# Kernel tuning notes

Hardware: AMD Instinct MI355X
Metric: run time of the kernel (lower is better)

The kernel has to match this reference:

```python
import jax, jax.numpy as jnp
import numpy as np

H = 12        # attention heads
WIN = 256     # one-sided sliding window (attention_window = 512)
L = 2         # encoder layers in this reference (full model: 12, same structure)
NEG = -1e9


def layer_norm(x, g, b, eps=1e-5):
    m = jnp.mean(x, axis=-1, keepdims=True)
    v = jnp.mean((x - m) ** 2, axis=-1, keepdims=True)
    return (x - m) * jax.lax.rsqrt(v + eps) * g + b


def heads(x):
    B, S, D = x.shape
    return x.reshape(B, S, H, D // H).transpose(0, 2, 1, 3)  # [B,H,S,Dh]


def overlap_chunks(x, w):
    # x: [B,H,S,D] -> [B,H,C,3w,D]; chunk c = keys/values seen by queries [c*w,(c+1)*w)
    B, Hh, S, D = x.shape
    xp = jnp.pad(x, ((0, 0), (0, 0), (w, w), (0, 0))).reshape(B, Hh, S // w + 2, w, D)
    return jnp.concatenate([xp[:, :, :-2], xp[:, :, 1:-1], xp[:, :, 2:]], axis=3)


def encoder_layer(x, mask, p):
    (Wq, bq, Wk, bk, Wv, bv, Wqg, bqg, Wkg, bkg, Wvg, bvg,
     Wo, bo, g1, b1n, W1, bf1, W2, bf2, g2, b2n) = p
    B, S, D = x.shape
    Dh = D // H
    w = WIN
    C = S // w
    scale = 1.0 / np.sqrt(Dh)
    q = heads(x @ Wq + bq)
    k = heads(x @ Wk + bk)
    v = heads(x @ Wv + bv)
    # --- sliding-window (banded) attention, chunked: each query chunk sees 3 key chunks ---
    qc = q.reshape(B, H, C, w, Dh)
    k3 = overlap_chunks(k, w)
    v3 = overlap_chunks(v, w)
    scores = jnp.einsum('bhcqd,bhckd->bhcqk', qc, k3) * scale  # [B,H,C,w,3w]
    qi = jnp.arange(w)[:, None]
    kr = jnp.arange(3 * w)[None, :] - w                       # key offset rel. to chunk start
    band = jnp.abs(kr - qi) <= w                              # [w,3w] |rel pos| <= w
    kpos = jnp.arange(C)[:, None] * w + (jnp.arange(3 * w) - w)[None, :]  # [C,3w] abs key idx
    inrange = (kpos >= 0) & (kpos < S)
    mp = jnp.pad(mask, ((0, 0), (w, w))).reshape(B, C + 2, w)
    m3 = jnp.concatenate([mp[:, :-2], mp[:, 1:-1], mp[:, 2:]], axis=2)  # [B,C,3w]
    loc_mask = band[None, :, :] & inrange[:, None, :]         # [C,w,3w]
    valid = loc_mask[None, None] & (m3 > 0)[:, None, :, None, :]
    scores = jnp.where(valid, scores, NEG)
    sloc = scores.reshape(B, H, S, 3 * w)
    # every token also attends to the global token (position 0)
    gsc = jnp.einsum('bhsd,bhd->bhs', q, k[:, :, 0]) * scale  # [B,H,S]
    attn = jax.nn.softmax(jnp.concatenate([sloc, gsc[..., None]], axis=-1), axis=-1)
    aloc = attn[..., :3 * w].reshape(B, H, C, w, 3 * w)
    ag = attn[..., -1]                                        # [B,H,S]
    out = jnp.einsum('bhcqk,bhckd->bhcqd', aloc, v3).reshape(B, H, S, Dh)
    out = out + ag[..., None] * v[:, :, 0][:, :, None, :]
    # --- global token full attention with separate global projections ---
    qg = heads(x @ Wqg + bqg)[:, :, 0]                        # [B,H,Dh]
    kg = heads(x @ Wkg + bkg)
    vg = heads(x @ Wvg + bvg)
    gs = jnp.where(mask[:, None, :] > 0,
                   jnp.einsum('bhd,bhsd->bhs', qg, kg) * scale, NEG)
    og = jnp.einsum('bhs,bhsd->bhd', jax.nn.softmax(gs, axis=-1), vg)
    out = out.at[:, :, 0].set(og)
    h = out.transpose(0, 2, 1, 3).reshape(B, S, D) @ Wo + bo
    x = layer_norm(x + h, g1, b1n)
    f = jax.nn.gelu(x @ W1 + bf1) @ W2 + bf2
    return layer_norm(x + f, g2, b2n)


def forward(input_ids, attention_mask, word_emb, pos_emb, ln_e_g, ln_e_b,
            Wq, bq, Wk, bk, Wv, bv, Wqg, bqg, Wkg, bkg, Wvg, bvg, Wo, bo,
            ln1_g, ln1_b, W1, bf1, W2, bf2, ln2_g, ln2_b, Wp, bp, Wc, bc):
    B, S = input_ids.shape
    x = word_emb[input_ids] + pos_emb[:S][None]
    x = layer_norm(x, ln_e_g, ln_e_b)
    for l in range(L):
        p = (Wq[l], bq[l], Wk[l], bk[l], Wv[l], bv[l], Wqg[l], bqg[l],
             Wkg[l], bkg[l], Wvg[l], bvg[l], Wo[l], bo[l], ln1_g[l], ln1_b[l],
             W1[l], bf1[l], W2[l], bf2[l], ln2_g[l], ln2_b[l])
        x = encoder_layer(x, attention_mask, p)
    pooled = jnp.tanh(x[:, 0] @ Wp + bp)   # BERT-style pooler on CLS
    return pooled @ Wc + bc


def setup_inputs() -> dict:
    B, S, D, V, F, NL = 2, 4096, 768, 50265, 3072, 2
    keys = iter(jax.random.split(jax.random.key(0), 64))
    def w(shape, s=0.02):
        return (jax.random.normal(next(keys), shape, jnp.float32) * s)
    inp = {
        'input_ids': jax.random.randint(next(keys), (B, S), 0, V),
        'attention_mask': jnp.ones((B, S), jnp.int32),
        'word_emb': w((V, D)), 'pos_emb': w((S, D)),
        'ln_e_g': jnp.ones((D,), jnp.float32), 'ln_e_b': jnp.zeros((D,), jnp.float32),
        'Wq': w((L, D, D)), 'bq': jnp.zeros((L, D), jnp.float32),
        'Wk': w((L, D, D)), 'bk': jnp.zeros((L, D), jnp.float32),
        'Wv': w((L, D, D)), 'bv': jnp.zeros((L, D), jnp.float32),
        'Wqg': w((L, D, D)), 'bqg': jnp.zeros((L, D), jnp.float32),
        'Wkg': w((L, D, D)), 'bkg': jnp.zeros((L, D), jnp.float32),
        'Wvg': w((L, D, D)), 'bvg': jnp.zeros((L, D), jnp.float32),
        'Wo': w((L, D, D)), 'bo': jnp.zeros((L, D), jnp.float32),
        'ln1_g': jnp.ones((L, D), jnp.float32), 'ln1_b': jnp.zeros((L, D), jnp.float32),
        'W1': w((L, D, F)), 'bf1': jnp.zeros((L, F), jnp.float32),
        'W2': w((L, F, D)), 'bf2': jnp.zeros((L, D), jnp.float32),
        'ln2_g': jnp.ones((L, D), jnp.float32), 'ln2_b': jnp.zeros((L, D), jnp.float32),
        'Wp': w((D, D)), 'bp': jnp.zeros((D,), jnp.float32),
        'Wc': w((D, NL)), 'bc': jnp.zeros((NL,), jnp.float32),
    }
    return inp


def reference(input_ids, attention_mask, word_emb, pos_emb, ln_e_g, ln_e_b,
              Wq, bq, Wk, bk, Wv, bv, Wqg, bqg, Wkg, bkg, Wvg, bvg, Wo, bo,
              ln1_g, ln1_b, W1, bf1, W2, bf2, ln2_g, ln2_b, Wp, bp, Wc, bc):
    return forward(input_ids, attention_mask, word_emb, pos_emb, ln_e_g, ln_e_b,
                   Wq, bq, Wk, bk, Wv, bv, Wqg, bqg, Wkg, bkg, Wvg, bvg, Wo, bo,
                   ln1_g, ln1_b, W1, bf1, W2, bf2, ln2_g, ln2_b, Wp, bp, Wc, bc)
```

## Files before the change

### kernel.cpp

```cpp
#include <hip/hip_runtime.h>
#include <hip/hip_bf16.h>
#include <math.h>

#define BB 2
#define SS 4096
#define DD 768
#define HH 12
#define DHH 64
#define WW 256
#define CC 16
#define FF 3072

typedef __attribute__((ext_vector_type(8))) short bf16x8;
typedef __attribute__((ext_vector_type(4))) float f32x4;

struct TP12 { const float* s[12]; unsigned short* d[12]; };
struct TP4  { const float* s[4];  unsigned short* d[4];  };

__device__ __forceinline__ float gelu_f(float x) {
    float u = 0.7978845608028654f * fmaf(0.044715f * x * x, x, x);
    return x / (1.f + __expf(-2.f * u));
}

__device__ __forceinline__ unsigned short bfb(float f) {
    __hip_bfloat16 h = __float2bfloat16(f);
    return *(unsigned short*)&h;
}

__device__ __forceinline__ float bf2f(unsigned short u) {
    return __uint_as_float(((unsigned int)u) << 16);
}

__device__ __forceinline__ void gload16(const void* g, void* l) {
    __builtin_amdgcn_global_load_lds(
        (const __attribute__((address_space(1))) unsigned int*)g,
        (__attribute__((address_space(3))) unsigned int*)l, 16, 0, 0);
}

__global__ __launch_bounds__(256) void transpose12_k(TP12 p)
{
    __shared__ float t[32][33];
    int z = blockIdx.z;
    const float* Wsrc = p.s[z];
    unsigned short* Wt = p.d[z];
    const int K = DD, N = DD;
    int n0 = blockIdx.x * 32, k0 = blockIdx.y * 32;
    int tx = threadIdx.x & 31, ty = threadIdx.x >> 5;
#pragma unroll
    for (int i = 0; i < 32; i += 8)
        t[ty + i][tx] = Wsrc[(size_t)(k0 + ty + i) * N + n0 + tx];
    __syncthreads();
#pragma unroll
    for (int i = 0; i < 32; i += 8)
        Wt[(size_t)(n0 + ty + i) * K + k0 + tx] = bfb(t[tx][ty + i]);
}

__global__ __launch_bounds__(256) void transposeR4_k(TP4 p)
{
    __shared__ float t[32][33];
    int z = blockIdx.z;
    const float* Wsrc = p.s[z];
    unsigned short* Wt = p.d[z];
    int K, N, n0, k0;
    if (z < 2) { K = DD; N = FF; n0 = blockIdx.x * 32; k0 = blockIdx.y * 32; }
    else { K = FF; N = DD; int cell = blockIdx.y * 96 + blockIdx.x;
           n0 = (cell % 24) * 32; k0 = (cell / 24) * 32; }
    int tx = threadIdx.x & 31, ty = threadIdx.x >> 5;
#pragma unroll
    for (int i = 0; i < 32; i += 8)
        t[ty + i][tx] = Wsrc[(size_t)(k0 + ty + i) * N + n0 + tx];
    __syncthreads();
#pragma unroll
    for (int i = 0; i < 32; i += 8)
        Wt[(size_t)(n0 + ty + i) * K + k0 + tx] = bfb(t[tx][ty + i]);
}

__global__ __launch_bounds__(256) void pack_bias5_k(const float* __restrict__ b0,
        const float* __restrict__ b1, const float* __restrict__ b2,
        const float* __restrict__ b3, const float* __restrict__ b4,
        float* __restrict__ dst)
{
    int gid = blockIdx.x * 256 + threadIdx.x;
    if (gid >= 2 * 5 * DD) return;
    int l = gid / (5 * DD), r = gid % (5 * DD), seg = r / DD, i = r % DD;
    const float* srcs[5] = { b0, b1, b2, b3, b4 };
    dst[gid] = srcs[seg][l * DD + i];
}

__global__ __launch_bounds__(256) void embed_ln_k(const int* __restrict__ ids,
        const float* __restrict__ wemb, const float* __restrict__ pemb,
        const float* __restrict__ g, const float* __restrict__ bta,
        float* __restrict__ x, unsigned short* __restrict__ xbf)
{
    int row = blockIdx.x;
    int s = row & (SS - 1);
    int tid = threadIdx.x;
    int lane = tid & 63, wvi = tid >> 6;
    __shared__ float red[8];
    float4 v = { 0.f, 0.f, 0.f, 0.f };
    if (tid < 192) {
        const float4* we = (const float4*)(wemb + (size_t)ids[row] * DD);
        const float4* pe = (const float4*)(pemb + (size_t)s * DD);
        float4 a = we[tid], b = pe[tid];
        v.x = a.x + b.x; v.y = a.y + b.y; v.z = a.z + b.z; v.w = a.w + b.w;
    }
    float sum = (v.x + v.y) + (v.z + v.w);
    float sq = fmaf(v.x, v.x, fmaf(v.y, v.y, fmaf(v.z, v.z, v.w * v.w)));
#pragma unroll
    for (int o = 1; o < 64; o <<= 1) {
        sum += __shfl_xor(sum, o);
        sq  += __shfl_xor(sq, o);
    }
    if (lane == 0) { red[wvi] = sum; red[4 + wvi] = sq; }
    __syncthreads();
    float S = (red[0] + red[1]) + (red[2] + red[3]);
    float Q = (red[4] + red[5]) + (red[6] + red[7]);
    float mean = S * (1.f / DD);
    float var = Q * (1.f / DD) - mean * mean;
    float rstd = rsqrtf(var + 1e-5f);
    if (tid < 192) {
        float4 gg = ((const float4*)g)[tid];
        float4 bb = ((const float4*)bta)[tid];
        float4 o;
        o.x = (v.x - mean) * rstd * gg.x + bb.x;
        o.y = (v.y - mean) * rstd * gg.y + bb.y;
        o.z = (v.z - mean) * rstd * gg.z + bb.z;
        o.w = (v.w - mean) * rstd * gg.w + bb.w;
        ((float4*)(x + (size_t)row * DD))[tid] = o;
        ushort4 ob = { bfb(o.x), bfb(o.y), bfb(o.z), bfb(o.w) };
        ((ushort4*)(xbf + (size_t)row * DD))[tid] = ob;
    }
}

__global__ __launch_bounds__(256) void add_ln_k(const float* __restrict__ xin,
        const float* __restrict__ hin, const float* __restrict__ g,
        const float* __restrict__ bta, float* __restrict__ xout,
        unsigned short* __restrict__ xbf)
{
    int row = blockIdx.x;
    int tid = threadIdx.x;
    int lane = tid & 63, wvi = tid >> 6;
    __shared__ float red[8];
    float4 v = { 0.f, 0.f, 0.f, 0.f };
    if (tid < 192) {
        float4 a = ((const float4*)(xin + (size_t)row * DD))[tid];
        float4 b = ((const float4*)(hin + (size_t)row * DD))[tid];
        v.x = a.x + b.x; v.y = a.y + b.y; v.z = a.z + b.z; v.w = a.w + b.w;
    }
    float sum = (v.x + v.y) + (v.z + v.w);
    float sq = fmaf(v.x, v.x, fmaf(v.y, v.y, fmaf(v.z, v.z, v.w * v.w)));
#pragma unroll
    for (int o = 1; o < 64; o <<= 1) {
        sum += __shfl_xor(sum, o);
        sq  += __shfl_xor(sq, o);
    }
    if (lane == 0) { red[wvi] = sum; red[4 + wvi] = sq; }
    __syncthreads();
    float S = (red[0] + red[1]) + (red[2] + red[3]);
    float Q = (red[4] + red[5]) + (red[6] + red[7]);
    float mean = S * (1.f / DD);
    float var = Q * (1.f / DD) - mean * mean;
    float rstd = rsqrtf(var + 1e-5f);
    if (tid < 192) {
        float4 gg = ((const float4*)g)[tid];
        float4 bb = ((const float4*)bta)[tid];
        float4 o;
        o.x = (v.x - mean) * rstd * gg.x + bb.x;
        o.y = (v.y - mean) * rstd * gg.y + bb.y;
        o.z = (v.z - mean) * rstd * gg.z + bb.z;
        o.w = (v.w - mean) * rstd * gg.w + bb.w;
        ((float4*)(xout + (size_t)row * DD))[tid] = o;
        ushort4 ob = { bfb(o.x), bfb(o.y), bfb(o.z), bfb(o.w) };
        ((ushort4*)(xbf + (size_t)row * DD))[tid] = ob;
    }
}

template<int OUT_BF16, int ACT_GELU>
__global__ __launch_bounds__(256) void mfma_gemm_k(
        const unsigned short* __restrict__ A,
        const unsigned short* __restrict__ Bt,
        const float* __restrict__ bias,
        void* __restrict__ Cv, int M, int N, int K)
{
    __shared__ short As[2 * 128 * 64];
    __shared__ short Bs[2 * 128 * 64];
    const int tid = threadIdx.x;
    const int lane = tid & 63, wv = tid >> 6;
    int nbx = gridDim.x;
    int nby = gridDim.y;
    int nwg = nbx * nby;
    int lid = blockIdx.y * nbx + blockIdx.x;
    int nid = ((nwg & 7) == 0) ? ((lid & 7) * (nwg >> 3) + (lid >> 3)) : lid;
    const int bm = (nid / nby) * 128, bn = (nid % nby) * 128;
    const int wm = wv >> 1, wn = wv & 1;

    const int srow0 = (tid * 16) >> 7;
    const int sbc   = (tid * 16) & 127;
    const int srcc  = sbc ^ ((srow0 & 7) << 4);
    const int ldst  = tid * 16;
    const char* Ab = (const char*)(A + (size_t)bm * K);
    const char* Bb = (const char*)(Bt + (size_t)bn * K);

    f32x4 acc[4][4];
#pragma unroll
    for (int i = 0; i < 4; i++)
#pragma unroll
        for (int j = 0; j < 4; j++) acc[i][j] = (f32x4){0.f, 0.f, 0.f, 0.f};

    const int lr = lane & 15;
    const int g = lane >> 4;
    const int rswz = (lr & 7) << 4;
    const int NK = K >> 6;

    auto stage = [&](int ib, int t) {
        const int k0 = t << 6;
        char* Ad = (char*)As + ib * 16384;
        char* Bd = (char*)Bs + ib * 16384;
#pragma unroll
        for (int p = 0; p < 4; p++) {
            size_t roff = (size_t)(srow0 + p * 32) * (K * 2) + (size_t)k0 * 2 + srcc;
            gload16(Ab + roff, Ad + p * 4096 + ldst);
            gload16(Bb + roff, Bd + p * 4096 + ldst);
        }
    };

    stage(0, 0);

    int cur = 0;
    for (int t = 0; t < NK; t++) {
        if (t + 1 < NK) {
            stage(cur ^ 1, t + 1);
            asm volatile("s_waitcnt vmcnt(8)" ::: "memory");
        } else {
            asm volatile("s_waitcnt vmcnt(0)" ::: "memory");
        }
        __builtin_amdgcn_sched_barrier(0);
        __builtin_amdgcn_s_barrier();
        __builtin_amdgcn_sched_barrier(0);

        const char* Ar = (const char*)As + cur * 16384;
        const char* Br = (const char*)Bs + cur * 16384;
#pragma unroll
        for (int kk = 0; kk < 2; kk++) {
            int colb = (kk * 64 + g * 16) ^ rswz;
            bf16x8 af[4], bfr[4];
#pragma unroll
            for (int i = 0; i < 4; i++)
                af[i] = *(const bf16x8*)(Ar + (wm * 64 + i * 16 + lr) * 128 + colb);
#pragma unroll
            for (int j = 0; j < 4; j++)
                bfr[j] = *(const bf16x8*)(Br + (wn * 64 + j * 16 + lr) * 128 + colb);
#pragma unroll
            for (int i = 0; i < 4; i++)
#pragma unroll
                for (int j = 0; j < 4; j++)
                    acc[i][j] = __builtin_amdgcn_mfma_f32_16x16x32_bf16(af[i], bfr[j], acc[i][j], 0, 0, 0);
        }
        __builtin_amdgcn_sched_barrier(0);
        __builtin_amdgcn_s_barrier();
        cur ^= 1;
    }

    const int rq = lane >> 4;
#pragma unroll
    for (int j = 0; j < 4; j++) {
        int col = bn + wn * 64 + j * 16 + lr;
        float bv = bias[col];
#pragma unroll
        for (int i = 0; i < 4; i++) {
            int rowb = bm + wm * 64 + i * 16 + rq * 4;
#pragma unroll
            for (int r = 0; r < 4; r++) {
                float o = acc[i][j][r] + bv;
                if (ACT_GELU) o = gelu_f(o);
                if (OUT_BF16)
                    ((unsigned short*)Cv)[(size_t)(rowb + r) * N + col] = bfb(o);
                else
                    ((float*)Cv)[(size_t)(rowb + r) * N + col] = o;
            }
        }
    }
}

__global__ __launch_bounds__(256) void vtrans_k(const unsigned short* __restrict__ packed,
        unsigned short* __restrict__ vt)
{
    int s0 = blockIdx.x * 64, h = blockIdx.y, b = blockIdx.z;
    int tid = threadIdx.x;
    __shared__ unsigned short t[64][72];
    int r = tid >> 3, dc = (tid & 7) * 8;
#pragma unroll
    for (int half = 0; half < 2; half++) {
        int rr = r + half * 32;
        const unsigned short* src = packed + (size_t)(b * SS + s0 + rr) * 3840 + 2 * DD + h * 64 + dc;
        *(uint4*)&t[rr][dc] = *(const uint4*)src;
    }
    __syncthreads();
    int d = tid >> 3, sc = (tid & 7) * 8;
#pragma unroll
    for (int half = 0; half < 2; half++) {
        int dd2 = d + half * 32;
        unsigned short v[8];
#pragma unroll
        for (int e = 0; e < 8; e++) v[e] = t[sc + e][dd2];
        unsigned short* dst = vt + (size_t)((b * HH + h) * 64 + dd2) * SS + s0 + sc;
        *(uint4*)dst = *(uint4*)v;
    }
}

__global__ __launch_bounds__(256) void swin_mfma_k(
        const unsigned short* __restrict__ packed,
        const unsigned short* __restrict__ vt,
        const int* __restrict__ mask,
        unsigned short* __restrict__ O)
{
    __shared__ __align__(16) char smem[52736];
    const int c2 = blockIdx.x, h = blockIdx.y, b = blockIdx.z;
    const int tid = threadIdx.x;
    const int lane = tid & 63, wv = tid >> 6;
    const int l15 = lane & 15, g = lane >> 4;
    const int bh = b * HH + h;
    const int q0 = c2 * 128;

    char* PB = smem + 32768 + wv * 4096;
    float* maskAll = (float*)(smem + 49152);
    float* sA = (float*)(smem + 51712);
    float* sB = (float*)(smem + 52224);

    const char* pk_bytes = (const char*)packed;
    const char* vt_bytes = (const char*)vt;

    bf16x8 qf[2][2];
#pragma unroll
    for (int j = 0; j < 2; j++)
#pragma unroll
        for (int kk = 0; kk < 2; kk++)
            qf[j][kk] = *(const bf16x8*)(packed +
                (size_t)(b * SS + q0 + wv * 32 + j * 16 + l15) * 3840 + h * 64 + kk * 32 + g * 8);
    bf16x8 gkf[2];
#pragma unroll
    for (int kk = 0; kk < 2; kk++)
        gkf[kk] = *(const bf16x8*)(packed + (size_t)(b * SS) * 3840 + DD + h * 64 + kk * 32 + g * 8);
    float v0r[4];
#pragma unroll
    for (int jd = 0; jd < 4; jd++)
        v0r[jd] = bf2f(vt[(size_t)(bh * 64 + jd * 16 + l15) * SS]);

    f32x4 o_[2][4];
#pragma unroll
    for (int i = 0; i < 2; i++)
#pragma unroll
        for (int j = 0; j < 4; j++) o_[i][j] = (f32x4){0.f, 0.f, 0.f, 0.f};
    float m_[2] = { -1e20f, -1e20f };
    float l_[2] = { 0.f, 0.f };

    const int rswz = (l15 & 7) << 4;
    const int kt_s = max(0, 4 - 2 * c2);
    const int kt_e = min(10, 68 - 2 * c2);
    const int lo = wv >> 1;

    auto stage = [&](int ib, int kt) {
        const int kpos0 = q0 - 256 + kt * 64;
        char* KTd = smem + ib * 8192;
        char* VTd = smem + 16384 + ib * 8192;
        int off = tid * 16;
#pragma unroll
        for (int ch = 0; ch < 2; ch++) {
            int o2 = off + ch * 4096;
            int row = o2 >> 7, bc = o2 & 127;
            int srcc = bc ^ ((row & 7) << 4);
            gload16(pk_bytes + (size_t)(b * SS + kpos0 + row) * 7680 + 1536 + h * 128 + srcc,
                    KTd + o2);
            gload16(vt_bytes + (size_t)(bh * 64 + row) * 8192 + (size_t)(kpos0 * 2 + srcc),
                    VTd + o2);
        }
    };

    stage(0, kt_s);
    {
        int span = (kt_e - kt_s) * 64;
        int base_k = q0 - 256 + kt_s * 64;
        for (int idx = tid; idx < span; idx += 256) {
            int kp = base_k + idx;
            maskAll[kt_s * 64 + idx] = (mask[b * SS + kp] > 0) ? 0.f : -1e30f;
        }
    }
    __syncthreads();

    int cur = 0;
    for (int kt = kt_s; kt < kt_e; kt++) {
        if (kt + 1 < kt_e) stage(cur ^ 1, kt + 1);

        const int dl = kt - lo;
        if (dl >= 0 && dl <= 8) {
            const char* KT = smem + cur * 8192;
            const char* VT = smem + 16384 + cur * 8192;
            const bool edge = (dl == 0) || (dl == 8);

            f32x4 mrd[4];
#pragma unroll
            for (int i = 0; i < 4; i++)
                mrd[i] = *(const f32x4*)&maskAll[kt * 64 + i * 16 + g * 4];

            f32x4 s_[4][2];
#pragma unroll
            for (int i = 0; i < 4; i++)
#pragma unroll
                for (int j = 0; j < 2; j++) s_[i][j] = (f32x4){0.f, 0.f, 0.f, 0.f};
            __builtin_amdgcn_s_setprio(1);
#pragma unroll
            for (int kk = 0; kk < 2; kk++) {
                bf16x8 af[4];
#pragma unroll
                for (int i = 0; i < 4; i++)
                    af[i] = *(const bf16x8*)(KT + (i * 16 + l15) * 128 + ((kk * 64 + g * 16) ^ rswz));
#pragma unroll
                for (int i = 0; i < 4; i++)
#pragma unroll
                    for (int j = 0; j < 2; j++)
                        s_[i][j] = __builtin_amdgcn_mfma_f32_16x16x32_bf16(af[i], qf[j][kk], s_[i][j], 0, 0, 0);
            }
            __builtin_amdgcn_s_setprio(0);

#pragma unroll
            for (int j = 0; j < 2; j++) {
                float tm = -1e30f;
                if (edge) {
#pragma unroll
                    for (int i = 0; i < 4; i++) {
#pragma unroll
                        for (int r = 0; r < 4; r++) {
                            float v = fmaf(s_[i][j][r], 0.125f, mrd[i][r]);
                            int rel = kt * 64 - 256 + i * 16 + g * 4 + r - wv * 32 - j * 16 - l15;
                            v = (rel > 256 || rel < -256) ? -1e30f : v;
                            s_[i][j][r] = v;
                            tm = fmaxf(tm, v);
                        }
                    }
                } else {
#pragma unroll
                    for (int i = 0; i < 4; i++) {
#pragma unroll
                        for (int r = 0; r < 4; r++) {
                            float v = fmaf(s_[i][j][r], 0.125f, mrd[i][r]);
                            s_[i][j][r] = v;
                            tm = fmaxf(tm, v);
                        }
                    }
                }
                tm = fmaxf(tm, __shfl_xor(tm, 16));
                tm = fmaxf(tm, __shfl_xor(tm, 32));
                float mn = fmaxf(m_[j], tm);
                float fac = __expf(m_[j] - mn);
                m_[j] = mn;
                float ls = 0.f;
                int q32 = j * 16 + l15;
#pragma unroll
                for (int i = 0; i < 4; i++) {
                    float p0 = __expf(s_[i][j][0] - mn);
                    float p1 = __expf(s_[i][j][1] - mn);
                    float p2 = __expf(s_[i][j][2] - mn);
                    float p3 = __expf(s_[i][j][3] - mn);
                    ls += (p0 + p1) + (p2 + p3);
                    uint2 pw;
                    pw.x = (unsigned int)bfb(p0) | ((unsigned int)bfb(p1) << 16);
                    pw.y = (unsigned int)bfb(p2) | ((unsigned int)bfb(p3) << 16);
                    *(uint2*)(PB + q32 * 128 + ((i * 32 + g * 8) ^ rswz)) = pw;
                }
                ls += __shfl_xor(ls, 16);
                ls += __shfl_xor(ls, 32);
                l_[j] = l_[j] * fac + ls;
                if (g == 0) sA[wv * 32 + q32] = fac;
            }

#pragma unroll
            for (int iq = 0; iq < 2; iq++) {
                f32x4 fc = *(const f32x4*)&sA[wv * 32 + iq * 16 + g * 4];
#pragma unroll
                for (int jd = 0; jd < 4; jd++)
#pragma unroll
                    for (int r = 0; r < 4; r++) o_[iq][jd][r] *= fc[r];
            }
            __builtin_amdgcn_s_setprio(1);
#pragma unroll
            for (int kk = 0; kk < 2; kk++) {
                bf16x8 pa[2], vb[4];
#pragma unroll
                for (int iq = 0; iq < 2; iq++)
                    pa[iq] = *(const bf16x8*)(PB + (iq * 16 + l15) * 128 + ((kk * 64 + g * 16) ^ rswz));
#pragma unroll
                for (int jd = 0; jd < 4; jd++)
                    vb[jd] = *(const bf16x8*)(VT + (jd * 16 + l15) * 128 + ((kk * 64 + g * 16) ^ rswz));
#pragma unroll
                for (int iq = 0; iq < 2; iq++)
#pragma unroll
                    for (int jd = 0; jd < 4; jd++)
                        o_[iq][jd] = __builtin_amdgcn_mfma_f32_16x16x32_bf16(pa[iq], vb[jd], o_[iq][jd], 0, 0, 0);
            }
            __builtin_amdgcn_s_setprio(0);
        }

        asm volatile("s_waitcnt vmcnt(0)" ::: "memory");
        __builtin_amdgcn_sched_barrier(0);
        __builtin_amdgcn_s_barrier();
        __builtin_amdgcn_sched_barrier(0);
        cur ^= 1;
    }

#pragma unroll
    for (int j = 0; j < 2; j++) {
        float pd = 0.f;
#pragma unroll
        for (int kk = 0; kk < 2; kk++)
#pragma unroll
            for (int e = 0; e < 8; e++)
                pd += bf2f((unsigned short)qf[j][kk][e]) * bf2f((unsigned short)gkf[kk][e]);
        pd += __shfl_xor(pd, 16);
        pd += __shfl_xor(pd, 32);
        float sg = pd * 0.125f;
        float mf = fmaxf(m_[j], sg);
        float fac = __expf(m_[j] - mf);
        float pg = __expf(sg - mf);
        float lf = l_[j] * fac + pg;
        float inv = 1.f / lf;
        if (g == 0) {
            sA[wv * 32 + j * 16 + l15] = fac * inv;
            sB[wv * 32 + j * 16 + l15] = pg * inv;
        }
    }
#pragma unroll
    for (int iq = 0; iq < 2; iq++) {
        f32x4 fA = *(const f32x4*)&sA[wv * 32 + iq * 16 + g * 4];
        f32x4 fB = *(const f32x4*)&sB[wv * 32 + iq * 16 + g * 4];
#pragma unroll
        for (int jd = 0; jd < 4; jd++) {
#pragma unroll
            for (int r = 0; r < 4; r++) {
                float val = o_[iq][jd][r] * fA[r] + fB[r] * v0r[jd];
                int row = b * SS + q0 + wv * 32 + iq * 16 + g * 4 + r;
                O[(size_t)row * DD + h * 64 + jd * 16 + l15] = bfb(val);
            }
        }
    }
}

__global__ __launch_bounds__(256) void gattn1_k(const float* __restrict__ qg,
        const unsigned short* __restrict__ packed, const int* __restrict__ mask,
        float* __restrict__ pm, float* __restrict__ pl, float* __restrict__ po)
{
    int cc = blockIdx.x, h = blockIdx.y, b = blockIdx.z;
    int tid = threadIdx.x;
    __shared__ float qs[64], red[256], ps[256], ored[4][64];
    if (tid < 64) qs[tid] = qg[b * DD + h * 64 + tid];
    __syncthreads();
    int s = cc * 256 + tid;
    const unsigned short* kr = packed + (size_t)(b * SS + s) * 3840 + 3 * DD + h * 64;
    float a = 0.f;
#pragma unroll
    for (int d8 = 0; d8 < 8; d8++) {
        bf16x8 kv = *(const bf16x8*)(kr + d8 * 8);
#pragma unroll
        for (int e = 0; e < 8; e++)
            a = fmaf(qs[d8 * 8 + e], bf2f((unsigned short)kv[e]), a);
    }
    a *= 0.125f;
    float sv = (mask[b * SS + s] > 0) ? a : -1e9f;
    red[tid] = sv; __syncthreads();
    for (int o = 128; o > 0; o >>= 1) {
        if (tid < o) red[tid] = fmaxf(red[tid], red[tid + o]);
        __syncthreads();
    }
    float mx = red[0]; __syncthreads();
    float p = __expf(sv - mx);
    ps[tid] = p;
    red[tid] = p; __syncthreads();
    for (int o = 128; o > 0; o >>= 1) {
        if (tid < o) red[tid] += red[tid + o];
        __syncthreads();
    }
    float ls = red[0];
    int d = tid & 63, grp = tid >> 6;
    const unsigned short* vgb = packed + 4 * DD + h * 64 + d;
    float oa = 0.f;
    for (int t = 0; t < 64; t++) {
        int srow = cc * 256 + grp * 64 + t;
        oa = fmaf(ps[grp * 64 + t], bf2f(vgb[(size_t)(b * SS + srow) * 3840]), oa);
    }
    ored[grp][d] = oa; __syncthreads();
    if (tid < 64) {
        int idx = (b * HH + h) * 16 + cc;
        po[(size_t)idx * 64 + tid] = ored[0][tid] + ored[1][tid] + ored[2][tid] + ored[3][tid];
        if (tid == 0) { pm[idx] = mx; pl[idx] = ls; }
    }
}

__global__ __launch_bounds__(64) void gattn2_k(const float* __restrict__ pm,
        const float* __restrict__ pl, const float* __restrict__ po,
        unsigned short* __restrict__ O)
{
    int h = blockIdx.x, b = blockIdx.y;
    int tid = threadIdx.x;
    int base = (b * HH + h) * 16;
    float mx = -1e30f;
    for (int c2 = 0; c2 < 16; c2++) mx = fmaxf(mx, pm[base + c2]);
    float den = 0.f, oa = 0.f;
    for (int c2 = 0; c2 < 16; c2++) {
        float w = __expf(pm[base + c2] - mx);
        den = fmaf(pl[base + c2], w, den);
        oa = fmaf(po[(size_t)(base + c2) * 64 + tid], w, oa);
    }
    O[(size_t)(b * SS) * DD + h * 64 + tid] = bfb(oa / den);
}

template<int ACT_TANH>
__global__ __launch_bounds__(256) void rowgemv_k(const float* __restrict__ x,
        size_t xstride, const float* __restrict__ W, const float* __restrict__ bias,
        float* __restrict__ dst, int N)
{
    int b = blockIdx.y;
    int colL = threadIdx.x & 63, part = threadIdx.x >> 6;
    int col = blockIdx.x * 64 + colL;
    __shared__ float partial[4][64];
    const float* xr = x + (size_t)b * xstride;
    float a = 0.f;
    for (int k = part * (DD / 4); k < (part + 1) * (DD / 4); k++)
        a = fmaf(xr[k], W[(size_t)k * N + col], a);
    partial[part][colL] = a; __syncthreads();
    if (part == 0) {
        float s = partial[0][colL] + partial[1][colL] + partial[2][colL] + partial[3][colL]
                + bias[col];
        if (ACT_TANH) s = tanhf(s);
        dst[b * N + col] = s;
    }
}

__global__ __launch_bounds__(256) void cls_k(const float* __restrict__ pooled,
        const float* __restrict__ Wc, const float* __restrict__ bc,
        float* __restrict__ out)
{
    int lane = threadIdx.x & 63, pair = threadIdx.x >> 6;
    int b = pair >> 1, cls = pair & 1;
    float a = 0.f;
#pragma unroll
    for (int j = 0; j < 12; j++) {
        int k = lane + j * 64;
        a = fmaf(pooled[b * DD + k], Wc[k * 2 + cls], a);
    }
#pragma unroll
    for (int o = 1; o < 64; o <<= 1) a += __shfl_xor(a, o);
    if (lane == 0) out[b * 2 + cls] = a + bc[cls];
}

extern "C" void kernel_launch(void* const* d_in, const int* in_sizes, int n_in,
                              void* d_out, int out_size, void* d_ws, size_t ws_size,
                              hipStream_t stream) {
    const int*   input_ids = (const int*)d_in[0];
    const int*   amask     = (const int*)d_in[1];
    const float* word_emb  = (const float*)d_in[2];
    const float* pos_emb   = (const float*)d_in[3];
    const float* ln_e_g    = (const float*)d_in[4];
    const float* ln_e_b    = (const float*)d_in[5];
    const float* Wq  = (const float*)d_in[6];  const float* bq  = (const float*)d_in[7];
    const float* Wk  = (const float*)d_in[8];  const float* bk  = (const float*)d_in[9];
    const float* Wv  = (const float*)d_in[10]; const float* bv  = (const float*)d_in[11];
    const float* Wqg = (const float*)d_in[12]; const float* bqg = (const float*)d_in[13];
    const float* Wkg = (const float*)d_in[14]; const float* bkg = (const float*)d_in[15];
    const float* Wvg = (const float*)d_in[16]; const float* bvg = (const float*)d_in[17];
    const float* Wo  = (const float*)d_in[18]; const float* bo  = (const float*)d_in[19];
    const float* ln1_g = (const float*)d_in[20]; const float* ln1_b = (const float*)d_in[21];
    const float* W1  = (const float*)d_in[22]; const float* bf1 = (const float*)d_in[23];
    const float* W2  = (const float*)d_in[24]; const float* bf2 = (const float*)d_in[25];
    const float* ln2_g = (const float*)d_in[26]; const float* ln2_b = (const float*)d_in[27];
    const float* Wp  = (const float*)d_in[28]; const float* bp  = (const float*)d_in[29];
    const float* Wc  = (const float*)d_in[30]; const float* bc  = (const float*)d_in[31];
    float* out = (float*)d_out;

    char* wsb = (char*)d_ws;
    float*          x      = (float*)(wsb + 0);
    unsigned short* xbf    = (unsigned short*)(wsb + 25165824);
    unsigned short* packed = (unsigned short*)(wsb + 37748736);
    unsigned short* vtb    = (unsigned short*)(wsb + 100663296);
    unsigned short* aout   = (unsigned short*)(wsb + 113246208);
    float*          hf     = (float*)(wsb + 125829120);
    char*           wts    = wsb + 150994944;
    float*          b5     = (float*)(wsb + 184025088);
    float*          qg     = (float*)(wsb + 184055808);
    float*          pm     = (float*)(wsb + 184061952);
    float*          pl     = (float*)(wsb + 184063488);
    float*          po     = (float*)(wsb + 184065024);
    float*          pooled = (float*)(wsb + 184163328);
    unsigned short* mid    = packed;

    const size_t SQ = (size_t)DD * DD;
    const size_t PER_L = (6 * SQ + 2 * (size_t)DD * FF) * 2;
    unsigned short* Wt5[2], *Wo_t[2], *W1_t[2], *W2_t[2];
    for (int l = 0; l < 2; l++) {
        char* base = wts + (size_t)l * PER_L;
        Wt5[l]  = (unsigned short*)base;
        Wo_t[l] = (unsigned short*)(base + 5 * SQ * 2);
        W1_t[l] = (unsigned short*)(base + 6 * SQ * 2);
        W2_t[l] = (unsigned short*)(base + 6 * SQ * 2 + (size_t)DD * FF * 2);
    }

    const int M = BB * SS;

    TP12 t12;
    for (int l = 0; l < 2; l++) {
        t12.s[l * 6 + 0] = Wq  + (size_t)l * SQ;  t12.d[l * 6 + 0] = Wt5[l] + 0 * SQ;
        t12.s[l * 6 + 1] = Wk  + (size_t)l * SQ;  t12.d[l * 6 + 1] = Wt5[l] + 1 * SQ;
        t12.s[l * 6 + 2] = Wv  + (size_t)l * SQ;  t12.d[l * 6 + 2] = Wt5[l] + 2 * SQ;
        t12.s[l * 6 + 3] = Wkg + (size_t)l * SQ;  t12.d[l * 6 + 3] = Wt5[l] + 3 * SQ;
        t12.s[l * 6 + 4] = Wvg + (size_t)l * SQ;  t12.d[l * 6 + 4] = Wt5[l] + 4 * SQ;
        t12.s[l * 6 + 5] = Wo  + (size_t)l * SQ;  t12.d[l * 6 + 5] = Wo_t[l];
    }
    TP4 t4;
    t4.s[0] = W1;                      t4.d[0] = W1_t[0];
    t4.s[1] = W1 + (size_t)DD * FF;    t4.d[1] = W1_t[1];
    t4.s[2] = W2;                      t4.d[2] = W2_t[0];
    t4.s[3] = W2 + (size_t)FF * DD;    t4.d[3] = W2_t[1];

    transpose12_k<<<dim3(24, 24, 12), 256, 0, stream>>>(t12);
    transposeR4_k<<<dim3(96, 24, 4), 256, 0, stream>>>(t4);
    pack_bias5_k<<<(2 * 5 * DD + 255) / 256, 256, 0, stream>>>(bq, bk, bv, bkg, bvg, b5);

    embed_ln_k<<<M, 256, 0, stream>>>(input_ids, word_emb, pos_emb, ln_e_g, ln_e_b, x, xbf);

    dim3 gqkv(M / 128, 3840 / 128);
    dim3 g768(M / 128, DD / 128);
    dim3 g3072(M / 128, FF / 128);

    for (int l = 0; l < 2; l++) {
        const float* Wqg_l = Wqg + (size_t)l * SQ; const float* bqg_l = bqg + (size_t)l * DD;
        const float* bo_l  = bo  + (size_t)l * DD;
        const float* bf1_l = bf1 + (size_t)l * FF;
        const float* bf2_l = bf2 + (size_t)l * DD;
        const float* g1_l  = ln1_g + (size_t)l * DD; const float* b1_l = ln1_b + (size_t)l * DD;
        const float* g2_l  = ln2_g + (size_t)l * DD; const float* b2_l = ln2_b + (size_t)l * DD;

        mfma_gemm_k<1, 0><<<gqkv, 256, 0, stream>>>(xbf, Wt5[l], b5 + (size_t)l * 3840,
                                                    packed, M, 3840, DD);
        vtrans_k<<<dim3(SS / 64, HH, BB), 256, 0, stream>>>(packed, vtb);
        rowgemv_k<0><<<dim3(DD / 64, BB), 256, 0, stream>>>(x, (size_t)SS * DD, Wqg_l, bqg_l, qg, DD);

        swin_mfma_k<<<dim3(SS / 128, HH, BB), 256, 0, stream>>>(packed, vtb, amask, aout);
        gattn1_k<<<dim3(16, HH, BB), 256, 0, stream>>>(qg, packed, amask, pm, pl, po);
        gattn2_k<<<dim3(HH, BB), 64, 0, stream>>>(pm, pl, po, aout);

        mfma_gemm_k<0, 0><<<g768, 256, 0, stream>>>(aout, Wo_t[l], bo_l, hf, M, DD, DD);
        add_ln_k<<<M, 256, 0, stream>>>(x, hf, g1_l, b1_l, x, xbf);

        mfma_gemm_k<1, 1><<<g3072, 256, 0, stream>>>(xbf, W1_t[l], bf1_l, mid, M, FF, DD);
        mfma_gemm_k<0, 0><<<g768, 256, 0, stream>>>(mid, W2_t[l], bf2_l, hf, M, DD, FF);
        add_ln_k<<<M, 256, 0, stream>>>(x, hf, g2_l, b2_l, x, xbf);
    }

    rowgemv_k<1><<<dim3(DD / 64, BB), 256, 0, stream>>>(x, (size_t)SS * DD, Wp, bp, pooled, DD);
    cls_k<<<1, 256, 0, stream>>>(pooled, Wc, bc, out);
}
```

Measured before the change: 682.2 us.

## Add 256x256-tile MFMA GEMM for QKV and FFN1 projections

Adds a new bf16 MFMA GEMM kernel with 256x256 output tiles, 512 threads (8 waves, each computing 128x64), double-buffered LDS and XOR-swizzled loads. It is used for the wide QKV (N=3840) and FFN-up (N=3072) GEMMs instead of the 128x128 kernel. The larger tile raises arithmetic intensity and operand reuse per global load. In exchange it uses 128 KB of LDS per block and more accumulator registers, and launches fewer blocks (480 for QKV, 384 for FFN1), which may underfill the 256 CUs.

```diff
diff --git a/kernel.cpp b/kernel.cpp
--- a/kernel.cpp
+++ b/kernel.cpp
@@ -269,6 +269,112 @@
 #pragma unroll
         for (int i = 0; i < 4; i++) {
             int rowb = bm + wm * 64 + i * 16 + rq * 4;
+#pragma unroll
+            for (int r = 0; r < 4; r++) {
+                float o = acc[i][j][r] + bv;
+                if (ACT_GELU) o = gelu_f(o);
+                if (OUT_BF16)
+                    ((unsigned short*)Cv)[(size_t)(rowb + r) * N + col] = bfb(o);
+                else
+                    ((float*)Cv)[(size_t)(rowb + r) * N + col] = o;
+            }
+        }
+    }
+}
+
+template<int OUT_BF16, int ACT_GELU>
+__global__ __launch_bounds__(512, 2) void mfma_gemm256_k(
+        const unsigned short* __restrict__ A,
+        const unsigned short* __restrict__ Bt,
+        const float* __restrict__ bias,
+        void* __restrict__ Cv, int M, int N, int K)
+{
+    __shared__ short As[2 * 256 * 64];
+    __shared__ short Bs[2 * 256 * 64];
+    const int tid = threadIdx.x;
+    const int lane = tid & 63, wv = tid >> 6;
+    int nbx = gridDim.x;
+    int nby = gridDim.y;
+    int nwg = nbx * nby;
+    int lid = blockIdx.y * nbx + blockIdx.x;
+    int nid = ((nwg & 7) == 0) ? ((lid & 7) * (nwg >> 3) + (lid >> 3)) : lid;
+    const int bm = (nid / nby) * 256, bn = (nid % nby) * 256;
+    const int wm = wv >> 2, wn = wv & 3;
+
+    const int srow0 = (tid * 16) >> 7;
+    const int sbc   = (tid * 16) & 127;
+    const int srcc  = sbc ^ ((srow0 & 7) << 4);
+    const int ldst  = tid * 16;
+    const char* Ab = (const char*)(A + (size_t)bm * K);
+    const char* Bb = (const char*)(Bt + (size_t)bn * K);
+
+    f32x4 acc[8][4];
+#pragma unroll
+    for (int i = 0; i < 8; i++)
+#pragma unroll
+        for (int j = 0; j < 4; j++) acc[i][j] = (f32x4){0.f, 0.f, 0.f, 0.f};
+
+    const int lr = lane & 15;
+    const int g = lane >> 4;
+    const int rswz = (lr & 7) << 4;
+    const int NK = K >> 6;
+
+    auto stage = [&](int ib, int t) {
+        const int k0 = t << 6;
+        char* Ad = (char*)As + ib * 32768;
+        char* Bd = (char*)Bs + ib * 32768;
+#pragma unroll
+        for (int p = 0; p < 4; p++) {
+            size_t roff = (size_t)(srow0 + p * 64) * (K * 2) + (size_t)k0 * 2 + srcc;
+            gload16(Ab + roff, Ad + p * 8192 + ldst);
+            gload16(Bb + roff, Bd + p * 8192 + ldst);
+        }
+    };
+
+    stage(0, 0);
+
+    int cur = 0;
+    for (int t = 0; t < NK; t++) {
+        if (t + 1 < NK) {
+            stage(cur ^ 1, t + 1);
+            asm volatile("s_waitcnt vmcnt(8)" ::: "memory");
+        } else {
+            asm volatile("s_waitcnt vmcnt(0)" ::: "memory");
+        }
+        __builtin_amdgcn_sched_barrier(0);
+        __builtin_amdgcn_s_barrier();
+        __builtin_amdgcn_sched_barrier(0);
+
+        const char* Ar = (const char*)As + cur * 32768;
+        const char* Br = (const char*)Bs + cur * 32768;
+#pragma unroll
+        for (int kk = 0; kk < 2; kk++) {
+            int colb = (kk * 64 + g * 16) ^ rswz;
+            bf16x8 bfr[4];
+#pragma unroll
+            for (int j = 0; j < 4; j++)
+                bfr[j] = *(const bf16x8*)(Br + (wn * 64 + j * 16 + lr) * 128 + colb);
+#pragma unroll
+            for (int i = 0; i < 8; i++) {
+                bf16x8 af = *(const bf16x8*)(Ar + (wm * 128 + i * 16 + lr) * 128 + colb);
+#pragma unroll
+                for (int j = 0; j < 4; j++)
+                    acc[i][j] = __builtin_amdgcn_mfma_f32_16x16x32_bf16(af, bfr[j], acc[i][j], 0, 0, 0);
+            }
+        }
+        __builtin_amdgcn_sched_barrier(0);
+        __builtin_amdgcn_s_barrier();
+        cur ^= 1;
+    }
+
+    const int rq = lane >> 4;
+#pragma unroll
+    for (int j = 0; j < 4; j++) {
+        int col = bn + wn * 64 + j * 16 + lr;
+        float bv = bias[col];
+#pragma unroll
+        for (int i = 0; i < 8; i++) {
+            int rowb = bm + wm * 128 + i * 16 + rq * 4;
 #pragma unroll
             for (int r = 0; r < 4; r++) {
                 float o = acc[i][j][r] + bv;
@@ -725,9 +831,9 @@
 
     embed_ln_k<<<M, 256, 0, stream>>>(input_ids, word_emb, pos_emb, ln_e_g, ln_e_b, x, xbf);
 
-    dim3 gqkv(M / 128, 3840 / 128);
+    dim3 gqkv(M / 256, 3840 / 256);
     dim3 g768(M / 128, DD / 128);
-    dim3 g3072(M / 128, FF / 128);
+    dim3 g3072(M / 256, FF / 256);
 
     for (int l = 0; l < 2; l++) {
         const float* Wqg_l = Wqg + (size_t)l * SQ; const float* bqg_l = bqg + (size_t)l * DD;
@@ -737,8 +843,8 @@
         const float* g1_l  = ln1_g + (size_t)l * DD; const float* b1_l = ln1_b + (size_t)l * DD;
         const float* g2_l  = ln2_g + (size_t)l * DD; const float* b2_l = ln2_b + (size_t)l * DD;
 
-        mfma_gemm_k<1, 0><<<gqkv, 256, 0, stream>>>(xbf, Wt5[l], b5 + (size_t)l * 3840,
-                                                    packed, M, 3840, DD);
+        mfma_gemm256_k<1, 0><<<gqkv, 512, 0, stream>>>(xbf, Wt5[l], b5 + (size_t)l * 3840,
+                                                       packed, M, 3840, DD);
         vtrans_k<<<dim3(SS / 64, HH, BB), 256, 0, stream>>>(packed, vtb);
         rowgemv_k<0><<<dim3(DD / 64, BB), 256, 0, stream>>>(x, (size_t)SS * DD, Wqg_l, bqg_l, qg, DD);
 
@@ -749,7 +855,7 @@
         mfma_gemm_k<0, 0><<<g768, 256, 0, stream>>>(aout, Wo_t[l], bo_l, hf, M, DD, DD);
         add_ln_k<<<M, 256, 0, stream>>>(x, hf, g1_l, b1_l, x, xbf);
 
-        mfma_gemm_k<1, 1><<<g3072, 256, 0, stream>>>(xbf, W1_t[l], bf1_l, mid, M, FF, DD);
+        mfma_gemm256_k<1, 1><<<g3072, 512, 0, stream>>>(xbf, W1_t[l], bf1_l, mid, M, FF, DD);
         mfma_gemm_k<0, 0><<<g768, 256, 0, stream>>>(mid, W2_t[l], bf2_l, hf, M, DD, FF);
         add_ln_k<<<M, 256, 0, stream>>>(x, hf, g2_l, b2_l, x, xbf);
     }
```

New measurement: 708.1 us. 1.04x slower.
